# Kernel optimization log

Hardware: AMD Instinct MI355X
Metric: run time of the kernel (lower is better)

## Reference

```python
import jax, jax.numpy as jnp
import numpy as np

B, S, D, H, E, TOPK = 8, 1024, 512, 2048, 8, 2


def setup_inputs() -> dict:
    key = jax.random.key(0)
    ks = jax.random.split(key, 7)
    scale = 0.02
    return {
        "x": jax.random.normal(ks[0], (B, S, D), jnp.float32),
        "gate_w": jax.random.normal(ks[1], (D, E), jnp.float32) * scale,
        "gate_b": jnp.zeros((E,), jnp.float32),
        "w1": jax.random.normal(ks[2], (E, D, H), jnp.float32) * scale,
        "b1": jnp.zeros((E, H), jnp.float32),
        "w2": jax.random.normal(ks[3], (E, H, D), jnp.float32) * scale,
        "b2": jnp.zeros((E, D), jnp.float32),
    }


def reference(x, gate_w, gate_b, w1, b1, w2, b2):
    # ---- MoE transformer MLP (fastmoe FMoETransformerMLP, NaiveGate) ----
    xt = x.reshape(-1, D)                       # [T, D], T = B*S tokens
    logits = xt @ gate_w + gate_b               # [T, E]
    top_val, top_idx = jax.lax.top_k(logits, TOPK)  # [T, k]
    score = jax.nn.softmax(top_val, axis=-1)    # softmax over the k selected logits

    y = jnp.zeros_like(xt)
    # Loop over the small fixed expert set; each token's combine weight for
    # expert e is the sum of its top-k scores routed to e (0 if not selected).
    for e in range(E):
        w_tok = jnp.sum(score * (top_idx == e), axis=-1)        # [T]
        h = jax.nn.gelu(xt @ w1[e] + b1[e], approximate=False)  # [T, H]
        y = y + w_tok[:, None] * (h @ w2[e] + b2[e])            # [T, D]

    y = y.reshape(B, S, D)
    # Outer model: log_softmax over seq of channel-summed features
    return jax.nn.log_softmax(jnp.sum(y, axis=2), axis=1)       # [B, S]
```

## Files before the change

### kernel.cpp

```cpp
#include <hip/hip_runtime.h>
#include <hip/hip_bf16.h>
#include <math.h>

#define T_TOK 8192
#define DIM   512
#define NEXP  8
#define HID   2048
#define NBAT  8
#define SEQ   1024

typedef short  short8 __attribute__((ext_vector_type(8)));
typedef float  f32x4  __attribute__((ext_vector_type(4)));

__device__ __forceinline__ unsigned short f2bf(float f) {
    union { float f; unsigned int u; } v; v.f = f;
    unsigned int u = v.u;
    unsigned int r = u + 0x7FFFu + ((u >> 16) & 1u);
    return (unsigned short)(r >> 16);
}

__device__ __forceinline__ float gelu_f(float v) {
    float v2 = v * v;
    float w = v * (-2.302344f - 0.102955f * v2);
    return v / (1.f + __builtin_amdgcn_exp2f(w));
}

__global__ void prep_k(const float* __restrict__ w1, unsigned short* __restrict__ w1t,
                       const float* __restrict__ w2, const float* __restrict__ b2,
                       float* __restrict__ w2sum, float* __restrict__ b2sum,
                       int* __restrict__ counts) {
    int bid = blockIdx.x;
    int tid = threadIdx.x;
    int wave = tid >> 6, lane = tid & 63;
    if (bid < 2048) {
        __shared__ unsigned short tile[64][65];
        int e = bid >> 8, r = bid & 255;
        int d0 = (r & 7) * 64, h0 = (r >> 3) * 64;
        const float* src = w1 + (size_t)e * DIM * HID;
        #pragma unroll
        for (int pass = 0; pass < 4; ++pass) {
            int dr = pass * 16 + (tid >> 4);
            int hc = (tid & 15) * 4;
            float4 v = *(const float4*)(src + (size_t)(d0 + dr) * HID + h0 + hc);
            tile[hc + 0][dr] = f2bf(v.x);
            tile[hc + 1][dr] = f2bf(v.y);
            tile[hc + 2][dr] = f2bf(v.z);
            tile[hc + 3][dr] = f2bf(v.w);
        }
        __syncthreads();
        unsigned short* dst = w1t + (size_t)e * HID * DIM;
        #pragma unroll
        for (int pass = 0; pass < 4; ++pass) {
            int hr = pass * 16 + (tid >> 4);
            int dc = (tid & 15) * 4;
            ushort4 o;
            o.x = tile[hr][dc];     o.y = tile[hr][dc + 1];
            o.z = tile[hr][dc + 2]; o.w = tile[hr][dc + 3];
            *(ushort4*)(dst + (size_t)(h0 + hr) * DIM + d0 + dc) = o;
        }
    } else if (bid < 2048 + 4096) {
        int row = (bid - 2048) * 4 + wave;
        const float* p = w2 + (size_t)row * DIM;
        float4 a = *(const float4*)(p + lane * 4);
        float4 b = *(const float4*)(p + 256 + lane * 4);
        float s = a.x + a.y + a.z + a.w + b.x + b.y + b.z + b.w;
        #pragma unroll
        for (int off = 32; off >= 1; off >>= 1) s += __shfl_xor(s, off);
        if (lane == 0) w2sum[row] = s;
    } else {
        if (tid < 8) counts[tid] = 0;
        for (int r = wave; r < NEXP; r += 4) {
            const float* p = b2 + (size_t)r * DIM;
            float s = 0.f;
            for (int i = lane; i < DIM; i += 64) s += p[i];
            #pragma unroll
            for (int off = 32; off >= 1; off >>= 1) s += __shfl_xor(s, off);
            if (lane == 0) b2sum[r] = s;
        }
    }
}

__global__ void gate2_k(const float* __restrict__ x, const float* __restrict__ gw,
                        const float* __restrict__ gb, const float* __restrict__ b2sum,
                        unsigned short* __restrict__ xb,
                        int* __restrict__ eidx, float* __restrict__ esc0,
                        float* __restrict__ esc1, float* __restrict__ s_partial) {
    int wave = threadIdx.x >> 6, lane = threadIdx.x & 63;
    int t = blockIdx.x * 4 + wave;
    const float* xp = x + (size_t)t * DIM;
    unsigned short* xbp = xb + (size_t)t * DIM;
    float acc[8] = {0, 0, 0, 0, 0, 0, 0, 0};
    #pragma unroll
    for (int it = 0; it < 8; ++it) {
        int d = it * 64 + lane;
        float xv = xp[d];
        xbp[d] = f2bf(xv);
        float4 g0 = *(const float4*)(gw + d * 8);
        float4 g1 = *(const float4*)(gw + d * 8 + 4);
        acc[0] += xv * g0.x; acc[1] += xv * g0.y; acc[2] += xv * g0.z; acc[3] += xv * g0.w;
        acc[4] += xv * g1.x; acc[5] += xv * g1.y; acc[6] += xv * g1.z; acc[7] += xv * g1.w;
    }
    #pragma unroll
    for (int e = 0; e < 8; ++e) {
        float s = acc[e];
        #pragma unroll
        for (int off = 32; off >= 1; off >>= 1) s += __shfl_xor(s, off);
        acc[e] = s + gb[e];
    }
    float v0 = -1e30f, v1 = -1e30f; int i0 = 0, i1 = 0;
    #pragma unroll
    for (int e = 0; e < 8; ++e) {
        float v = acc[e];
        if (v > v0) { v1 = v0; i1 = i0; v0 = v; i0 = e; }
        else if (v > v1) { v1 = v; i1 = e; }
    }
    float e1 = expf(v1 - v0);
    float inv = 1.f / (1.f + e1);
    float s0 = inv, s1 = e1 * inv;
    if (lane == 0) {
        eidx[t] = i0 | (i1 << 4);
        esc0[t] = s0;
        esc1[t] = s1;
        s_partial[t] = s0 * b2sum[i0] + s1 * b2sum[i1];
    }
}

__global__ __launch_bounds__(1024) void route_k(
    const int* __restrict__ eidx, const float* __restrict__ esc0,
    const float* __restrict__ esc1, int* __restrict__ counts,
    int* __restrict__ ptok, float* __restrict__ pscore) {
    int tid = threadIdx.x;
    int t = blockIdx.x * 1024 + tid;
    int wv = tid >> 6, lane = tid & 63;
    int pk = eidx[t];
    int i0 = pk & 0xf, i1 = (pk >> 4) & 0xf;
    float s0 = esc0[t], s1 = esc1[t];

    __shared__ int waveCnt[16][8];
    __shared__ int waveBase[16][8];

    unsigned long long m0[8], m1[8];
    #pragma unroll
    for (int e = 0; e < 8; ++e) {
        m0[e] = __ballot(i0 == e);
        m1[e] = __ballot(i1 == e);
    }
    if (lane < 8) {
        int c = 0;
        #pragma unroll
        for (int e = 0; e < 8; ++e)
            if (lane == e) c = __popcll(m0[e]) + __popcll(m1[e]);
        waveCnt[wv][lane] = c;
    }
    __syncthreads();
    if (tid < 8) {
        int e = tid;
        int total = 0;
        #pragma unroll
        for (int w = 0; w < 16; ++w) total += waveCnt[w][e];
        int base = atomicAdd(&counts[e], total);
        int run = base;
        #pragma unroll
        for (int w = 0; w < 16; ++w) {
            waveBase[w][e] = run;
            run += waveCnt[w][e];
        }
    }
    __syncthreads();

    unsigned long long lt = (1ULL << lane) - 1ULL;
    int slot0 = 0, slot1 = 0;
    #pragma unroll
    for (int e = 0; e < 8; ++e) {
        if (i0 == e) slot0 = waveBase[wv][e] + __popcll(m0[e] & lt);
        if (i1 == e) slot1 = waveBase[wv][e] + __popcll(m0[e]) + __popcll(m1[e] & lt);
    }
    ptok[i0 * T_TOK + slot0] = t;  pscore[i0 * T_TOK + slot0] = s0;
    ptok[i1 * T_TOK + slot1] = t;  pscore[i1 * T_TOK + slot1] = s1;
}

#define GPTR(p) (const __attribute__((address_space(1))) void*)(p)
#define LPTR(p) (__attribute__((address_space(3))) void*)(p)

__global__ __launch_bounds__(256) void moe_gemm_k(
    const unsigned short* __restrict__ xb, const unsigned short* __restrict__ w1t,
    const float* __restrict__ b1, const float* __restrict__ w2sum,
    const int* __restrict__ counts, const int* __restrict__ ptok,
    const float* __restrict__ pscore, float* __restrict__ s_partial) {

    int bx = blockIdx.x;
    int e = 8, rowBase = 0, accT = 0;
    #pragma unroll
    for (int i = 0; i < 8; ++i) {
        int nt = (counts[i] + 127) >> 7;
        if (e == 8 && bx < accT + nt) { e = i; rowBase = (bx - accT) * 128; }
        accT += nt;
    }
    if (e == 8) return;
    int n_e = counts[e];
    int hBase = blockIdx.y * 128;

    __shared__ unsigned short A_s[128 * 64];
    __shared__ unsigned short B_s[128 * 64];
    __shared__ int   tokLds[128];
    __shared__ float scoreLds[128];

    int tid = threadIdx.x;
    int wave = tid >> 6, lane = tid & 63;

    if (tid < 128) {
        int r = rowBase + tid;
        bool valid = r < n_e;
        tokLds[tid]   = valid ? ptok[e * T_TOK + r]   : 0;
        scoreLds[tid] = valid ? pscore[e * T_TOK + r] : 0.f;
    }
    __syncthreads();

    const unsigned short* gA[4];
    const unsigned short* gB[4];
    int lo[4];
    #pragma unroll
    for (int i = 0; i < 4; ++i) {
        int c = (i * 4 + wave) * 64 + lane;
        int row = c >> 3, pos = c & 7;
        int j = (pos ^ (row & 7)) * 8;
        gA[i] = xb + (size_t)tokLds[row] * DIM + j;
        gB[i] = w1t + ((size_t)e * HID + hBase + row) * DIM + j;
        lo[i] = c * 8;
    }

    int wm = wave >> 1, wn = wave & 1;
    int quad = lane >> 4, col = lane & 15;

    f32x4 acc[4][4];
    #pragma unroll
    for (int m = 0; m < 4; ++m)
        #pragma unroll
        for (int n = 0; n < 4; ++n)
            acc[m][n] = (f32x4){0.f, 0.f, 0.f, 0.f};

    for (int kk = 0; kk < 8; ++kk) {
        __syncthreads();
        int ko = kk * 64;
        #pragma unroll
        for (int i = 0; i < 4; ++i) {
            __builtin_amdgcn_global_load_lds(GPTR(gA[i] + ko), LPTR(&A_s[lo[i]]), 16, 0, 0);
            __builtin_amdgcn_global_load_lds(GPTR(gB[i] + ko), LPTR(&B_s[lo[i]]), 16, 0, 0);
        }
        __syncthreads();
        #pragma unroll
        for (int kh = 0; kh < 2; ++kh) {
            int swz = (((kh << 2) | quad) ^ (col & 7)) * 8;
            const unsigned short* aB = A_s + (wm * 64 + col) * 64 + swz;
            const unsigned short* bB = B_s + (wn * 64 + col) * 64 + swz;
            short8 af[4], bf[4];
            #pragma unroll
            for (int m = 0; m < 4; ++m) af[m] = *(const short8*)(aB + m * 16 * 64);
            #pragma unroll
            for (int n = 0; n < 4; ++n) bf[n] = *(const short8*)(bB + n * 16 * 64);
            #pragma unroll
            for (int m = 0; m < 4; ++m)
                #pragma unroll
                for (int n = 0; n < 4; ++n)
                    acc[m][n] = __builtin_amdgcn_mfma_f32_16x16x32_bf16(af[m], bf[n], acc[m][n], 0, 0, 0);
        }
    }

    const float* b1e = b1 + e * HID;
    const float* w2e = w2sum + e * HID;
    float bias[4], wsum[4];
    #pragma unroll
    for (int n = 0; n < 4; ++n) {
        int h = hBase + wn * 64 + n * 16 + col;
        bias[n] = b1e[h];
        wsum[n] = w2e[h];
    }
    #pragma unroll
    for (int m = 0; m < 4; ++m) {
        float rp0 = 0.f, rp1 = 0.f, rp2 = 0.f, rp3 = 0.f;
        #pragma unroll
        for (int n = 0; n < 4; ++n) {
            rp0 += gelu_f(acc[m][n][0] + bias[n]) * wsum[n];
            rp1 += gelu_f(acc[m][n][1] + bias[n]) * wsum[n];
            rp2 += gelu_f(acc[m][n][2] + bias[n]) * wsum[n];
            rp3 += gelu_f(acc[m][n][3] + bias[n]) * wsum[n];
        }
        #pragma unroll
        for (int off = 8; off >= 1; off >>= 1) {
            rp0 += __shfl_xor(rp0, off);
            rp1 += __shfl_xor(rp1, off);
            rp2 += __shfl_xor(rp2, off);
            rp3 += __shfl_xor(rp3, off);
        }
        if (col < 4) {
            float mine = (col == 0) ? rp0 : (col == 1) ? rp1 : (col == 2) ? rp2 : rp3;
            int rl = wm * 64 + m * 16 + quad * 4 + col;
            int r = rowBase + rl;
            if (r < n_e)
                atomicAdd(&s_partial[tokLds[rl]], scoreLds[rl] * mine);
        }
    }
}

__global__ void lsm_k(const float* __restrict__ s, float* __restrict__ out) {
    int b = blockIdx.x, tid = threadIdx.x;
    int wave = tid >> 6, lane = tid & 63;
    __shared__ float red[4];
    const float* sp = s + (size_t)b * SEQ;
    float v[4];
    #pragma unroll
    for (int i = 0; i < 4; ++i) v[i] = sp[tid + i * 256];
    float m = fmaxf(fmaxf(v[0], v[1]), fmaxf(v[2], v[3]));
    #pragma unroll
    for (int off = 32; off >= 1; off >>= 1) m = fmaxf(m, __shfl_xor(m, off));
    if (lane == 0) red[wave] = m;
    __syncthreads();
    m = fmaxf(fmaxf(red[0], red[1]), fmaxf(red[2], red[3]));
    __syncthreads();
    float t = 0.f;
    #pragma unroll
    for (int i = 0; i < 4; ++i) t += expf(v[i] - m);
    #pragma unroll
    for (int off = 32; off >= 1; off >>= 1) t += __shfl_xor(t, off);
    if (lane == 0) red[wave] = t;
    __syncthreads();
    t = red[0] + red[1] + red[2] + red[3];
    float L = m + logf(t);
    #pragma unroll
    for (int i = 0; i < 4; ++i) out[(size_t)b * SEQ + tid + i * 256] = v[i] - L;
}

extern "C" void kernel_launch(void* const* d_in, const int* in_sizes, int n_in,
                              void* d_out, int out_size, void* d_ws, size_t ws_size,
                              hipStream_t stream) {
    const float* x  = (const float*)d_in[0];
    const float* gw = (const float*)d_in[1];
    const float* gb = (const float*)d_in[2];
    const float* w1 = (const float*)d_in[3];
    const float* b1 = (const float*)d_in[4];
    const float* w2 = (const float*)d_in[5];
    const float* b2 = (const float*)d_in[6];
    float* out = (float*)d_out;

    char* ws = (char*)d_ws;
    int*   counts    = (int*)  (ws + 0);
    float* b2sum     = (float*)(ws + 1280);
    float* s_partial = (float*)(ws + 1536);
    float* w2sum     = (float*)(ws + 34304);
    int*   ptok      = (int*)  (ws + 99840);
    float* pscore    = (float*)(ws + 361984);
    int*   eidx      = (int*)  (ws + 624128);
    float* esc0      = (float*)(ws + 656896);
    float* esc1      = (float*)(ws + 689664);
    unsigned short* xb  = (unsigned short*)(ws + 722432);
    unsigned short* w1t = (unsigned short*)(ws + 9111040);

    prep_k<<<2048 + 4096 + 1, 256, 0, stream>>>(w1, w1t, w2, b2, w2sum, b2sum, counts);
    gate2_k<<<T_TOK / 4, 256, 0, stream>>>(x, gw, gb, b2sum, xb, eidx, esc0, esc1, s_partial);
    route_k<<<NEXP, 1024, 0, stream>>>(eidx, esc0, esc1, counts, ptok, pscore);
    moe_gemm_k<<<dim3(135, 16), 256, 0, stream>>>(xb, w1t, b1, w2sum, counts, ptok, pscore, s_partial);
    lsm_k<<<NBAT, 256, 0, stream>>>(s_partial, out);
}
```

Before: 213.7 us.

## Fuse gating into prep kernel and widen GEMM tile to 128x256

The gate/top-k/bf16-conversion work moves into the prep kernel as extra blocks, removing one launch. The b2sum-based s_partial init moves into route_k, because b2sum is now computed in the same launch as gating. Each thread now loads 8 contiguous x values, with matching gate-weight indexing. The expert GEMM tile grows from 128x128 to 128x256 on the hidden dimension, halving the y-grid and reusing each A tile across more columns, at the cost of double the accumulator registers and larger LDS per block.

After: 242.8 us. +13.6%, slower.

```diff
diff --git a/kernel.cpp b/kernel.cpp
--- a/kernel.cpp
+++ b/kernel.cpp
@@ -25,7 +25,11 @@
     return v / (1.f + __builtin_amdgcn_exp2f(w));
 }
 
-__global__ void prep_k(const float* __restrict__ w1, unsigned short* __restrict__ w1t,
+__global__ void prep_k(const float* __restrict__ x, const float* __restrict__ gw,
+                       const float* __restrict__ gb, unsigned short* __restrict__ xb,
+                       int* __restrict__ eidx, float* __restrict__ esc0,
+                       float* __restrict__ esc1,
+                       const float* __restrict__ w1, unsigned short* __restrict__ w1t,
                        const float* __restrict__ w2, const float* __restrict__ b2,
                        float* __restrict__ w2sum, float* __restrict__ b2sum,
                        int* __restrict__ counts) {
@@ -33,8 +37,51 @@
     int tid = threadIdx.x;
     int wave = tid >> 6, lane = tid & 63;
     if (bid < 2048) {
+        int t = bid * 4 + wave;
+        const float* xp = x + (size_t)t * DIM + lane * 8;
+        float4 xa = *(const float4*)(xp);
+        float4 xc = *(const float4*)(xp + 4);
+        unsigned short pk8[8];
+        pk8[0] = f2bf(xa.x); pk8[1] = f2bf(xa.y); pk8[2] = f2bf(xa.z); pk8[3] = f2bf(xa.w);
+        pk8[4] = f2bf(xc.x); pk8[5] = f2bf(xc.y); pk8[6] = f2bf(xc.z); pk8[7] = f2bf(xc.w);
+        *(short8*)(xb + (size_t)t * DIM + lane * 8) = *(short8*)pk8;
+        float acc[8] = {0, 0, 0, 0, 0, 0, 0, 0};
+        const float* gwp = gw + lane * 8 * 8;
+        float xv[8] = {xa.x, xa.y, xa.z, xa.w, xc.x, xc.y, xc.z, xc.w};
+        #pragma unroll
+        for (int j = 0; j < 8; ++j) {
+            float4 g0 = *(const float4*)(gwp + j * 8);
+            float4 g1 = *(const float4*)(gwp + j * 8 + 4);
+            acc[0] += xv[j] * g0.x; acc[1] += xv[j] * g0.y;
+            acc[2] += xv[j] * g0.z; acc[3] += xv[j] * g0.w;
+            acc[4] += xv[j] * g1.x; acc[5] += xv[j] * g1.y;
+            acc[6] += xv[j] * g1.z; acc[7] += xv[j] * g1.w;
+        }
+        #pragma unroll
+        for (int e = 0; e < 8; ++e) {
+            float s = acc[e];
+            #pragma unroll
+            for (int off = 32; off >= 1; off >>= 1) s += __shfl_xor(s, off);
+            acc[e] = s + gb[e];
+        }
+        float v0 = -1e30f, v1 = -1e30f; int i0 = 0, i1 = 0;
+        #pragma unroll
+        for (int e = 0; e < 8; ++e) {
+            float v = acc[e];
+            if (v > v0) { v1 = v0; i1 = i0; v0 = v; i0 = e; }
+            else if (v > v1) { v1 = v; i1 = e; }
+        }
+        float e1 = expf(v1 - v0);
+        float inv = 1.f / (1.f + e1);
+        if (lane == 0) {
+            eidx[t] = i0 | (i1 << 4);
+            esc0[t] = inv;
+            esc1[t] = e1 * inv;
+        }
+    } else if (bid < 4096) {
         __shared__ unsigned short tile[64][65];
-        int e = bid >> 8, r = bid & 255;
+        int r = bid - 2048;
+        int e = r >> 8; r &= 255;
         int d0 = (r & 7) * 64, h0 = (r >> 3) * 64;
         const float* src = w1 + (size_t)e * DIM * HID;
         #pragma unroll
@@ -58,8 +105,8 @@
             o.z = tile[hr][dc + 2]; o.w = tile[hr][dc + 3];
             *(ushort4*)(dst + (size_t)(h0 + hr) * DIM + d0 + dc) = o;
         }
-    } else if (bid < 2048 + 4096) {
-        int row = (bid - 2048) * 4 + wave;
+    } else if (bid < 8192) {
+        int row = (bid - 4096) * 4 + wave;
         const float* p = w2 + (size_t)row * DIM;
         float4 a = *(const float4*)(p + lane * 4);
         float4 b = *(const float4*)(p + 256 + lane * 4);
@@ -80,61 +127,18 @@
     }
 }
 
-__global__ void gate2_k(const float* __restrict__ x, const float* __restrict__ gw,
-                        const float* __restrict__ gb, const float* __restrict__ b2sum,
-                        unsigned short* __restrict__ xb,
-                        int* __restrict__ eidx, float* __restrict__ esc0,
-                        float* __restrict__ esc1, float* __restrict__ s_partial) {
-    int wave = threadIdx.x >> 6, lane = threadIdx.x & 63;
-    int t = blockIdx.x * 4 + wave;
-    const float* xp = x + (size_t)t * DIM;
-    unsigned short* xbp = xb + (size_t)t * DIM;
-    float acc[8] = {0, 0, 0, 0, 0, 0, 0, 0};
-    #pragma unroll
-    for (int it = 0; it < 8; ++it) {
-        int d = it * 64 + lane;
-        float xv = xp[d];
-        xbp[d] = f2bf(xv);
-        float4 g0 = *(const float4*)(gw + d * 8);
-        float4 g1 = *(const float4*)(gw + d * 8 + 4);
-        acc[0] += xv * g0.x; acc[1] += xv * g0.y; acc[2] += xv * g0.z; acc[3] += xv * g0.w;
-        acc[4] += xv * g1.x; acc[5] += xv * g1.y; acc[6] += xv * g1.z; acc[7] += xv * g1.w;
-    }
-    #pragma unroll
-    for (int e = 0; e < 8; ++e) {
-        float s = acc[e];
-        #pragma unroll
-        for (int off = 32; off >= 1; off >>= 1) s += __shfl_xor(s, off);
-        acc[e] = s + gb[e];
-    }
-    float v0 = -1e30f, v1 = -1e30f; int i0 = 0, i1 = 0;
-    #pragma unroll
-    for (int e = 0; e < 8; ++e) {
-        float v = acc[e];
-        if (v > v0) { v1 = v0; i1 = i0; v0 = v; i0 = e; }
-        else if (v > v1) { v1 = v; i1 = e; }
-    }
-    float e1 = expf(v1 - v0);
-    float inv = 1.f / (1.f + e1);
-    float s0 = inv, s1 = e1 * inv;
-    if (lane == 0) {
-        eidx[t] = i0 | (i1 << 4);
-        esc0[t] = s0;
-        esc1[t] = s1;
-        s_partial[t] = s0 * b2sum[i0] + s1 * b2sum[i1];
-    }
-}
-
 __global__ __launch_bounds__(1024) void route_k(
     const int* __restrict__ eidx, const float* __restrict__ esc0,
-    const float* __restrict__ esc1, int* __restrict__ counts,
-    int* __restrict__ ptok, float* __restrict__ pscore) {
+    const float* __restrict__ esc1, const float* __restrict__ b2sum,
+    int* __restrict__ counts, int* __restrict__ ptok, float* __restrict__ pscore,
+    float* __restrict__ s_partial) {
     int tid = threadIdx.x;
     int t = blockIdx.x * 1024 + tid;
     int wv = tid >> 6, lane = tid & 63;
     int pk = eidx[t];
     int i0 = pk & 0xf, i1 = (pk >> 4) & 0xf;
     float s0 = esc0[t], s1 = esc1[t];
+    s_partial[t] = s0 * b2sum[i0] + s1 * b2sum[i1];
 
     __shared__ int waveCnt[16][8];
     __shared__ int waveBase[16][8];
@@ -198,10 +202,10 @@
     }
     if (e == 8) return;
     int n_e = counts[e];
-    int hBase = blockIdx.y * 128;
+    int hBase = blockIdx.y * 256;
 
     __shared__ unsigned short A_s[128 * 64];
-    __shared__ unsigned short B_s[128 * 64];
+    __shared__ unsigned short B_s[256 * 64];
     __shared__ int   tokLds[128];
     __shared__ float scoreLds[128];
 
@@ -216,62 +220,69 @@
     }
     __syncthreads();
 
-    const unsigned short* gA[4];
-    const unsigned short* gB[4];
-    int lo[4];
+    const unsigned short* gA[4]; int loA[4];
     #pragma unroll
     for (int i = 0; i < 4; ++i) {
-        int c = (i * 4 + wave) * 64 + lane;
-        int row = c >> 3, pos = c & 7;
-        int j = (pos ^ (row & 7)) * 8;
+        int c = i * 256 + tid;
+        int row = c >> 3;
+        int j = ((c & 7) ^ (row & 7)) * 8;
         gA[i] = xb + (size_t)tokLds[row] * DIM + j;
+        loA[i] = c * 8;
+    }
+    const unsigned short* gB[8]; int loB[8];
+    #pragma unroll
+    for (int i = 0; i < 8; ++i) {
+        int c = i * 256 + tid;
+        int row = c >> 3;
+        int j = ((c & 7) ^ (row & 7)) * 8;
         gB[i] = w1t + ((size_t)e * HID + hBase + row) * DIM + j;
-        lo[i] = c * 8;
+        loB[i] = c * 8;
     }
 
     int wm = wave >> 1, wn = wave & 1;
     int quad = lane >> 4, col = lane & 15;
 
-    f32x4 acc[4][4];
+    f32x4 acc[4][8];
     #pragma unroll
     for (int m = 0; m < 4; ++m)
         #pragma unroll
-        for (int n = 0; n < 4; ++n)
+        for (int n = 0; n < 8; ++n)
             acc[m][n] = (f32x4){0.f, 0.f, 0.f, 0.f};
 
     for (int kk = 0; kk < 8; ++kk) {
         __syncthreads();
         int ko = kk * 64;
         #pragma unroll
-        for (int i = 0; i < 4; ++i) {
-            __builtin_amdgcn_global_load_lds(GPTR(gA[i] + ko), LPTR(&A_s[lo[i]]), 16, 0, 0);
-            __builtin_amdgcn_global_load_lds(GPTR(gB[i] + ko), LPTR(&B_s[lo[i]]), 16, 0, 0);
-        }
+        for (int i = 0; i < 4; ++i)
+            __builtin_amdgcn_global_load_lds(GPTR(gA[i] + ko), LPTR(&A_s[loA[i]]), 16, 0, 0);
+        #pragma unroll
+        for (int i = 0; i < 8; ++i)
+            __builtin_amdgcn_global_load_lds(GPTR(gB[i] + ko), LPTR(&B_s[loB[i]]), 16, 0, 0);
         __syncthreads();
         #pragma unroll
         for (int kh = 0; kh < 2; ++kh) {
             int swz = (((kh << 2) | quad) ^ (col & 7)) * 8;
             const unsigned short* aB = A_s + (wm * 64 + col) * 64 + swz;
-            const unsigned short* bB = B_s + (wn * 64 + col) * 64 + swz;
-            short8 af[4], bf[4];
+            const unsigned short* bB = B_s + (wn * 128 + col) * 64 + swz;
+            short8 af[4], bf[8];
             #pragma unroll
             for (int m = 0; m < 4; ++m) af[m] = *(const short8*)(aB + m * 16 * 64);
             #pragma unroll
-            for (int n = 0; n < 4; ++n) bf[n] = *(const short8*)(bB + n * 16 * 64);
+            for (int n = 0; n < 8; ++n) bf[n] = *(const short8*)(bB + n * 16 * 64);
             #pragma unroll
             for (int m = 0; m < 4; ++m)
                 #pragma unroll
-                for (int n = 0; n < 4; ++n)
+                for (int n = 0; n < 8; ++n)
                     acc[m][n] = __builtin_amdgcn_mfma_f32_16x16x32_bf16(af[m], bf[n], acc[m][n], 0, 0, 0);
         }
     }
 
     const float* b1e = b1 + e * HID;
     const float* w2e = w2sum + e * HID;
-    float bias[4], wsum[4];
-    #pragma unroll
-    for (int n = 0; n < 4; ++n) {
-        int h = hBase + wn * 64 + n * 16 + col;
+    float bias[8], wsum[8];
+    #pragma unroll
+    for (int n = 0; n < 8; ++n) {
+        int h = hBase + wn * 128 + n * 16 + col;
         bias[n] = b1e[h];
         wsum[n] = w2e[h];
     }
@@ -279,7 +290,7 @@
     for (int m = 0; m < 4; ++m) {
         float rp0 = 0.f, rp1 = 0.f, rp2 = 0.f, rp3 = 0.f;
         #pragma unroll
-        for (int n = 0; n < 4; ++n) {
+        for (int n = 0; n < 8; ++n) {
             rp0 += gelu_f(acc[m][n][0] + bias[n]) * wsum[n];
             rp1 += gelu_f(acc[m][n][1] + bias[n]) * wsum[n];
             rp2 += gelu_f(acc[m][n][2] + bias[n]) * wsum[n];
@@ -355,9 +366,9 @@
     unsigned short* xb  = (unsigned short*)(ws + 722432);
     unsigned short* w1t = (unsigned short*)(ws + 9111040);
 
-    prep_k<<<2048 + 4096 + 1, 256, 0, stream>>>(w1, w1t, w2, b2, w2sum, b2sum, counts);
-    gate2_k<<<T_TOK / 4, 256, 0, stream>>>(x, gw, gb, b2sum, xb, eidx, esc0, esc1, s_partial);
-    route_k<<<NEXP, 1024, 0, stream>>>(eidx, esc0, esc1, counts, ptok, pscore);
-    moe_gemm_k<<<dim3(135, 16), 256, 0, stream>>>(xb, w1t, b1, w2sum, counts, ptok, pscore, s_partial);
+    prep_k<<<8193, 256, 0, stream>>>(x, gw, gb, xb, eidx, esc0, esc1,
+                                     w1, w1t, w2, b2, w2sum, b2sum, counts);
+    route_k<<<NEXP, 1024, 0, stream>>>(eidx, esc0, esc1, b2sum, counts, ptok, pscore, s_partial);
+    moe_gemm_k<<<dim3(135, 8), 256, 0, stream>>>(xb, w1t, b1, w2sum, counts, ptok, pscore, s_partial);
     lsm_k<<<NBAT, 256, 0, stream>>>(s_partial, out);
 }
```
